# Kernel tuning notes

Hardware: AMD Instinct MI355X
Metric: run time of the kernel (lower is better)

The kernel has to match this reference:

```python
import jax, jax.numpy as jnp
import numpy as np

NEG_INF = jnp.float32(-(2.0**32) + 1.0)


def squash(z):
    # z: [B, k_max, out_units]
    sq_norm = jnp.sum(jnp.square(z), axis=-1, keepdims=True)
    scale = sq_norm / (1.0 + sq_norm) / jnp.sqrt(sq_norm + 1e-8)
    return scale * z


def setup_inputs() -> dict:
    key = jax.random.key(0)
    k1, k2, k3, k4 = jax.random.split(key, 4)
    B, L, D_IN, D_OUT, K = 1024, 200, 256, 256, 8
    behavior_embeddings = jax.random.normal(k1, (B, L, D_IN), dtype=jnp.float32)
    seq_len = jax.random.randint(k2, (B, 1), 1, L + 1, dtype=jnp.int32)
    routing_logits = jax.random.normal(k3, (1, K, L), dtype=jnp.float32)  # init_std=1.0
    bilinear_mapping_matrix = jax.random.normal(k4, (D_IN, D_OUT), dtype=jnp.float32)
    return {
        "behavior_embeddings": behavior_embeddings,
        "seq_len": seq_len,
        "routing_logits": routing_logits,
        "bilinear_mapping_matrix": bilinear_mapping_matrix,
    }


def reference(behavior_embeddings, seq_len, routing_logits, bilinear_mapping_matrix):
    ITERATION_TIMES = 3
    B, L, _ = behavior_embeddings.shape
    K = routing_logits.shape[1]

    # mask: [B, 1, L] broadcastable to [B, K, L] (same seq_len for every capsule)
    mask = jnp.arange(L)[None, None, :] < seq_len[:, :, None]

    # bilinear map is loop-invariant: [B, L, out_units]
    mapped = jnp.einsum("ble,eo->blo", behavior_embeddings, bilinear_mapping_matrix)

    logits = routing_logits  # [1, K, L]
    interest_capsules = None
    for _ in range(ITERATION_TIMES):
        logits_pad = jnp.where(mask, jnp.broadcast_to(logits, (B, K, L)), NEG_INF)
        weight = jax.nn.softmax(logits_pad, axis=-1)          # [B, K, L]
        Z = jnp.einsum("bkl,blo->bko", weight, mapped)         # [B, K, out]
        interest_capsules = squash(Z)                          # [B, K, out]
        # delta: sum over batch of capsules @ mapped^T -> [1, K, L]
        delta = jnp.einsum("bko,blo->kl", interest_capsules, mapped)[None]
        logits = logits + delta  # emulates assign_add on non-trainable B

    return interest_capsules.reshape(-1, K, interest_capsules.shape[-1])
```

## Files before the change

kernel.cpp:

```cpp
#include <hip/hip_runtime.h>
#include <cstdint>
#include <cstddef>

#define B_    1024
#define L_    200
#define DIN_  256
#define DOUT_ 256
#define K_    8
#define M_    (B_ * L_)

typedef __attribute__((ext_vector_type(8))) short bf16x8;
typedef __attribute__((ext_vector_type(4))) float f32x4;

__device__ __forceinline__ float bf2f(unsigned short u) {
  union { unsigned int i; float f; } w; w.i = ((unsigned int)u) << 16; return w.f;
}
__device__ __forceinline__ unsigned short f2bf(float f) {
  union { float f; unsigned int i; } w; w.f = f;
  unsigned int x = w.i;
  return (unsigned short)((x + 0x7fffu + ((x >> 16) & 1u)) >> 16);
}

__global__ __launch_bounds__(256)
void wt_prep(const float* __restrict__ W, unsigned short* __restrict__ Wh,
             unsigned short* __restrict__ Wm, unsigned short* __restrict__ Wl)
{
  const int k = blockIdx.x;
  const int n = threadIdx.x;
  float x = W[k * DOUT_ + n];
  unsigned short h = f2bf(x);
  float r = x - bf2f(h);
  unsigned short m = f2bf(r);
  float r2 = r - bf2f(m);
  unsigned short l = f2bf(r2);
  const int k0b = k >> 5, quad = (k >> 3) & 3, j = k & 7;
  const int nt = n >> 4, lr = n & 15;
  const size_t idx = ((((size_t)k0b * 16 + nt) * 64) + (quad * 16 + lr)) * 8 + j;
  Wh[idx] = h;
  Wm[idx] = m;
  Wl[idx] = l;
}

__global__ __launch_bounds__(256, 2)
void gemm_mapped(const float* __restrict__ A,
                 const unsigned short* __restrict__ Wh,
                 const unsigned short* __restrict__ Wm,
                 const unsigned short* __restrict__ Wl,
                 float* __restrict__ C)
{
  const int t    = threadIdx.x;
  const int wave = t >> 6;
  const int lane = t & 63;
  const int quad = lane >> 4;
  const int lr   = lane & 15;
  const int m0   = blockIdx.x * 128 + wave * 32;

  f32x4 acc[2][16];
  #pragma unroll
  for (int mt = 0; mt < 2; ++mt)
    #pragma unroll
    for (int nt = 0; nt < 16; ++nt)
      acc[mt][nt] = (f32x4){0.f, 0.f, 0.f, 0.f};

  bf16x8 Bh[4], Bm[4], Bl[4];
  bf16x8 ah[2], am[2], al[2];
  float4 Af[2][2];

#define BLOAD(K0B, NT, S) do { \
    const size_t _off = (((size_t)(K0B) * 16 + (NT)) * 64 + lane) * 8; \
    Bh[S] = *(const bf16x8*)(Wh + _off); \
    Bm[S] = *(const bf16x8*)(Wm + _off); \
    Bl[S] = *(const bf16x8*)(Wl + _off); \
  } while (0)

  const float* ap0 = A + (size_t)(m0 + lr) * DIN_ + quad * 8;
  const float* ap1 = A + (size_t)(m0 + 16 + lr) * DIN_ + quad * 8;

  Af[0][0] = *(const float4*)(ap0);
  Af[0][1] = *(const float4*)(ap0 + 4);
  Af[1][0] = *(const float4*)(ap1);
  Af[1][1] = *(const float4*)(ap1 + 4);
  BLOAD(0, 0, 0); BLOAD(0, 1, 1); BLOAD(0, 2, 2); BLOAD(0, 3, 3);

  for (int k0b = 0; k0b < 8; ++k0b) {
    #pragma unroll
    for (int mt = 0; mt < 2; ++mt) {
      float xs[8] = {Af[mt][0].x, Af[mt][0].y, Af[mt][0].z, Af[mt][0].w,
                     Af[mt][1].x, Af[mt][1].y, Af[mt][1].z, Af[mt][1].w};
      #pragma unroll
      for (int j = 0; j < 8; ++j) {
        unsigned short h = f2bf(xs[j]);
        float r = xs[j] - bf2f(h);
        unsigned short mm = f2bf(r);
        float r2 = r - bf2f(mm);
        unsigned short ll = f2bf(r2);
        ah[mt][j] = (short)h; am[mt][j] = (short)mm; al[mt][j] = (short)ll;
      }
    }
    if (k0b < 7) {
      const int ko = (k0b + 1) * 32;
      Af[0][0] = *(const float4*)(ap0 + ko);
      Af[0][1] = *(const float4*)(ap0 + ko + 4);
      Af[1][0] = *(const float4*)(ap1 + ko);
      Af[1][1] = *(const float4*)(ap1 + ko + 4);
    }

#define GROUP(NT, S) do { \
    f32x4 c0 = acc[0][NT], c1 = acc[1][NT]; \
    c0 = __builtin_amdgcn_mfma_f32_16x16x32_bf16(ah[0], Bh[S], c0, 0, 0, 0); \
    c1 = __builtin_amdgcn_mfma_f32_16x16x32_bf16(ah[1], Bh[S], c1, 0, 0, 0); \
    c0 = __builtin_amdgcn_mfma_f32_16x16x32_bf16(ah[0], Bm[S], c0, 0, 0, 0); \
    c1 = __builtin_amdgcn_mfma_f32_16x16x32_bf16(ah[1], Bm[S], c1, 0, 0, 0); \
    c0 = __builtin_amdgcn_mfma_f32_16x16x32_bf16(am[0], Bh[S], c0, 0, 0, 0); \
    c1 = __builtin_amdgcn_mfma_f32_16x16x32_bf16(am[1], Bh[S], c1, 0, 0, 0); \
    c0 = __builtin_amdgcn_mfma_f32_16x16x32_bf16(ah[0], Bl[S], c0, 0, 0, 0); \
    c1 = __builtin_amdgcn_mfma_f32_16x16x32_bf16(ah[1], Bl[S], c1, 0, 0, 0); \
    c0 = __builtin_amdgcn_mfma_f32_16x16x32_bf16(am[0], Bm[S], c0, 0, 0, 0); \
    c1 = __builtin_amdgcn_mfma_f32_16x16x32_bf16(am[1], Bm[S], c1, 0, 0, 0); \
    c0 = __builtin_amdgcn_mfma_f32_16x16x32_bf16(al[0], Bh[S], c0, 0, 0, 0); \
    c1 = __builtin_amdgcn_mfma_f32_16x16x32_bf16(al[1], Bh[S], c1, 0, 0, 0); \
    acc[0][NT] = c0; acc[1][NT] = c1; \
  } while (0)

    GROUP(0, 0);  BLOAD(k0b, 4, 0);
    GROUP(1, 1);  BLOAD(k0b, 5, 1);
    GROUP(2, 2);  BLOAD(k0b, 6, 2);
    GROUP(3, 3);  BLOAD(k0b, 7, 3);
    GROUP(4, 0);  BLOAD(k0b, 8, 0);
    GROUP(5, 1);  BLOAD(k0b, 9, 1);
    GROUP(6, 2);  BLOAD(k0b, 10, 2);
    GROUP(7, 3);  BLOAD(k0b, 11, 3);
    GROUP(8, 0);  BLOAD(k0b, 12, 0);
    GROUP(9, 1);  BLOAD(k0b, 13, 1);
    GROUP(10, 2); BLOAD(k0b, 14, 2);
    GROUP(11, 3); BLOAD(k0b, 15, 3);
    GROUP(12, 0);
    GROUP(13, 1);
    GROUP(14, 2);
    GROUP(15, 3);
    if (k0b < 7) {
      BLOAD(k0b + 1, 0, 0); BLOAD(k0b + 1, 1, 1);
      BLOAD(k0b + 1, 2, 2); BLOAD(k0b + 1, 3, 3);
    }
#undef GROUP
  }
#undef BLOAD

  #pragma unroll
  for (int mt = 0; mt < 2; ++mt)
    #pragma unroll
    for (int nt = 0; nt < 16; ++nt)
      #pragma unroll
      for (int r = 0; r < 4; ++r) {
        int row = m0 + mt * 16 + quad * 4 + r;
        C[(size_t)row * DOUT_ + nt * 16 + lr] = acc[mt][nt][r];
      }
}

#define DSCALE     67108864.0f
#define DSCALE_INV 1.4901161193847656e-8f

__global__ __launch_bounds__(256, 4)
void z_soft(const float* __restrict__ mapped,
            const float* __restrict__ rlog,
            const long long* __restrict__ accA,
            const long long* __restrict__ accB,
            const int* __restrict__ seq_len,
            float* __restrict__ caps)
{
  const int t    = threadIdx.x;
  const int lane = t & 63;
  const int wave = t >> 6;
  const int b    = blockIdx.x;
  const int len  = seq_len[b];

  __shared__ float wsmT[200][8];
  __shared__ float zred[2][8][256];
  __shared__ float sqred[4][8];

  #pragma unroll
  for (int kk = 0; kk < 2; ++kk) {
    const int k = wave * 2 + kk;
    float v[4];
    float mx = -3.4028235e38f;
    #pragma unroll
    for (int i = 0; i < 4; ++i) {
      int l = lane + 64 * i;
      float lv = -3.4028235e38f;
      if (l < len) {
        long long a = accA[(k * L_ + l) * 8] + accB[(k * L_ + l) * 8];
        lv = rlog[k * L_ + l] + (float)a * DSCALE_INV;
      }
      v[i] = lv;
      mx = fmaxf(mx, lv);
    }
    #pragma unroll
    for (int s = 1; s < 64; s <<= 1) mx = fmaxf(mx, __shfl_xor(mx, s, 64));
    float e[4]; float sum = 0.f;
    #pragma unroll
    for (int i = 0; i < 4; ++i) {
      int l = lane + 64 * i;
      e[i] = (l < len) ? __expf(v[i] - mx) : 0.f;
      sum += e[i];
    }
    #pragma unroll
    for (int s = 1; s < 64; s <<= 1) sum += __shfl_xor(sum, s, 64);
    float inv = 1.f / sum;
    #pragma unroll
    for (int i = 0; i < 4; ++i) {
      int l = lane + 64 * i;
      if (l < L_) wsmT[l][k] = e[i] * inv;
    }
  }
  __syncthreads();

  f32x4 zacc[K_];
  #pragma unroll
  for (int k = 0; k < K_; ++k) zacc[k] = (f32x4){0.f, 0.f, 0.f, 0.f};

  const float* mp = mapped + (size_t)b * (L_ * DOUT_) + lane * 4;
  for (int l = wave; l < len; l += 4) {
    f32x4 m = *(const f32x4*)(mp + (size_t)l * DOUT_);
    float4 w0 = *(const float4*)&wsmT[l][0];
    float4 w1 = *(const float4*)&wsmT[l][4];
    zacc[0] += w0.x * m; zacc[1] += w0.y * m;
    zacc[2] += w0.z * m; zacc[3] += w0.w * m;
    zacc[4] += w1.x * m; zacc[5] += w1.y * m;
    zacc[6] += w1.z * m; zacc[7] += w1.w * m;
  }

  if (wave >= 2) {
    #pragma unroll
    for (int k = 0; k < K_; ++k)
      *(f32x4*)&zred[wave - 2][k][lane * 4] = zacc[k];
  }
  __syncthreads();
  if (wave < 2) {
    #pragma unroll
    for (int k = 0; k < K_; ++k) {
      f32x4 r = *(const f32x4*)&zred[wave][k][lane * 4];
      r += zacc[k];
      *(f32x4*)&zred[wave][k][lane * 4] = r;
    }
  }
  __syncthreads();

  float z[K_];
  #pragma unroll
  for (int k = 0; k < K_; ++k) z[k] = zred[0][k][t] + zred[1][k][t];

  #pragma unroll
  for (int k = 0; k < K_; ++k) {
    float s2 = z[k] * z[k];
    #pragma unroll
    for (int s = 1; s < 64; s <<= 1) s2 += __shfl_xor(s2, s, 64);
    if (lane == 0) sqred[wave][k] = s2;
  }
  __syncthreads();
  #pragma unroll
  for (int k = 0; k < K_; ++k) {
    float sq = sqred[0][k] + sqred[1][k] + sqred[2][k] + sqred[3][k];
    float scale = sq / ((1.f + sq) * sqrtf(sq + 1e-8f));
    caps[((size_t)b * K_ + k) * DOUT_ + t] = scale * z[k];
  }
}

__global__ __launch_bounds__(256)
void delta_kernel(const float* __restrict__ mapped, const float* __restrict__ caps,
                  long long* __restrict__ accOut)
{
  const int t    = threadIdx.x;
  const int lane = t & 63;
  const int wave = t >> 6;
  const int wid  = blockIdx.x * 4 + wave;
  const int lc   = wid % 50;
  const int bc   = wid / 50;
  const int l0   = lc * 4;
  const int o4   = lane * 4;

  const float* cb = caps   + (size_t)(bc * 16) * (K_ * DOUT_) + o4;
  const float* mb = mapped + ((size_t)(bc * 16) * L_ + l0) * DOUT_ + o4;

  float acc[K_][4];
  #pragma unroll
  for (int k = 0; k < K_; ++k)
    #pragma unroll
    for (int ll = 0; ll < 4; ++ll) acc[k][ll] = 0.f;

  float4 cA[K_], mA[4], cB[K_], mB[4];

#define LOADC(DST, BI) do { \
    const float* _p = cb + (size_t)(BI) * (K_ * DOUT_); \
    _Pragma("unroll") \
    for (int _k = 0; _k < K_; ++_k) DST[_k] = *(const float4*)(_p + _k * DOUT_); \
  } while (0)
#define LOADM(DST, BI) do { \
    const float* _p = mb + (size_t)(BI) * (L_ * DOUT_); \
    _Pragma("unroll") \
    for (int _l = 0; _l < 4; ++_l) DST[_l] = *(const float4*)(_p + _l * DOUT_); \
  } while (0)
#define COMPUTE(CC, MM) do { \
    _Pragma("unroll") \
    for (int _k = 0; _k < K_; ++_k) \
      _Pragma("unroll") \
      for (int _l = 0; _l < 4; ++_l) \
        acc[_k][_l] += CC[_k].x * MM[_l].x + CC[_k].y * MM[_l].y \
                     + CC[_k].z * MM[_l].z + CC[_k].w * MM[_l].w; \
  } while (0)

  LOADC(cA, 0); LOADM(mA, 0);
  for (int i = 0; i < 8; ++i) {
    LOADC(cB, 2 * i + 1); LOADM(mB, 2 * i + 1);
    COMPUTE(cA, mA);
    if (i < 7) { LOADC(cA, 2 * i + 2); LOADM(mA, 2 * i + 2); }
    COMPUTE(cB, mB);
  }
#undef LOADC
#undef LOADM
#undef COMPUTE

  float out = 0.f;
  #pragma unroll
  for (int k = 0; k < K_; ++k)
    #pragma unroll
    for (int ll = 0; ll < 4; ++ll) {
      float v = acc[k][ll];
      v += __shfl_xor(v, 1, 64);
      v += __shfl_xor(v, 2, 64);
      v += __shfl_xor(v, 4, 64);
      v += __shfl_xor(v, 8, 64);
      v += __shfl_xor(v, 16, 64);
      v += __shfl_xor(v, 32, 64);
      if (lane == k * 4 + ll) out = v;
    }
  if (lane < 32) {
    long long q = llrintf(out * DSCALE);
    atomicAdd((unsigned long long*)&accOut[((size_t)(lane >> 2) * L_ + l0 + (lane & 3)) * 8],
              (unsigned long long)q);
  }
}

__global__ __launch_bounds__(256)
void init_acc(long long* __restrict__ a)
{
  int i = blockIdx.x * 256 + threadIdx.x;
  a[i] = 0;
}

extern "C" void kernel_launch(void* const* d_in, const int* in_sizes, int n_in,
                              void* d_out, int out_size, void* d_ws, size_t ws_size,
                              hipStream_t stream)
{
  const float* behav = (const float*)d_in[0];
  const int*   slen  = (const int*)d_in[1];
  const float* rlog  = (const float*)d_in[2];
  const float* W     = (const float*)d_in[3];
  float* caps = (float*)d_out;

  char* ws = (char*)d_ws;
  long long* z0   = (long long*)ws;
  long long* acc0 = (long long*)(ws + 102400);
  long long* acc1 = (long long*)(ws + 204800);
  unsigned short* Wh = (unsigned short*)(ws + 327680);
  unsigned short* Wm = (unsigned short*)(ws + 458752);
  unsigned short* Wl = (unsigned short*)(ws + 589824);
  float* mapped   = (float*)(ws + (1 << 20));

  init_acc<<<dim3(150), 256, 0, stream>>>((long long*)ws);
  wt_prep<<<dim3(256), 256, 0, stream>>>(W, Wh, Wm, Wl);
  gemm_mapped<<<dim3(1600), 256, 0, stream>>>(behav, Wh, Wm, Wl, mapped);

  z_soft<<<dim3(B_), 256, 0, stream>>>(mapped, rlog, z0,   z0,   slen, caps);
  delta_kernel<<<dim3(800), 256, 0, stream>>>(mapped, caps, acc0);
  z_soft<<<dim3(B_), 256, 0, stream>>>(mapped, rlog, acc0, z0,   slen, caps);
  delta_kernel<<<dim3(800), 256, 0, stream>>>(mapped, caps, acc1);
  z_soft<<<dim3(B_), 256, 0, stream>>>(mapped, rlog, acc0, acc1, slen, caps);
}
```

Baseline: 606.1 us.

## Stage split-bf16 weight tiles in LDS via async loads and split N across waves

The GEMM now loads each K-slice of the three bf16 weight splits into shared memory with global_load_lds, shared by all four waves, instead of each wave reading B directly from global memory. Waves are now split 2x2 over M and N, so each wave computes 32 rows by 128 columns, the block covers 64 rows, and the grid doubles. This cuts redundant global and L2 traffic for the weights and lowers accumulator registers so occupancy can rise. The cost is a full barrier with vmcnt(0) per K-step and no double buffering, so load latency is exposed, and the A-side conversion work is duplicated across the two N-halves.

```diff
diff --git a/kernel.cpp b/kernel.cpp
--- a/kernel.cpp
+++ b/kernel.cpp
@@ -19,6 +19,12 @@
   union { float f; unsigned int i; } w; w.f = f;
   unsigned int x = w.i;
   return (unsigned short)((x + 0x7fffu + ((x >> 16) & 1u)) >> 16);
+}
+
+__device__ __forceinline__ void gload16(const void* g, void* l) {
+  __builtin_amdgcn_global_load_lds(
+      (const __attribute__((address_space(1))) unsigned int*)g,
+      (__attribute__((address_space(3))) unsigned int*)l, 16, 0, 0);
 }
 
 __global__ __launch_bounds__(256)
@@ -41,7 +47,7 @@
   Wl[idx] = l;
 }
 
-__global__ __launch_bounds__(256, 2)
+__global__ __launch_bounds__(256, 3)
 void gemm_mapped(const float* __restrict__ A,
                  const unsigned short* __restrict__ Wh,
                  const unsigned short* __restrict__ Wm,
@@ -53,34 +59,41 @@
   const int lane = t & 63;
   const int quad = lane >> 4;
   const int lr   = lane & 15;
-  const int m0   = blockIdx.x * 128 + wave * 32;
-
-  f32x4 acc[2][16];
+  const int m0   = blockIdx.x * 64 + (wave & 1) * 32;
+  const int nt0  = (wave >> 1) * 8;
+
+  __shared__ unsigned short ldsB[3 * 16 * 64 * 8];
+
+  f32x4 acc[2][8];
   #pragma unroll
   for (int mt = 0; mt < 2; ++mt)
     #pragma unroll
-    for (int nt = 0; nt < 16; ++nt)
+    for (int nt = 0; nt < 8; ++nt)
       acc[mt][nt] = (f32x4){0.f, 0.f, 0.f, 0.f};
 
-  bf16x8 Bh[4], Bm[4], Bl[4];
   bf16x8 ah[2], am[2], al[2];
   float4 Af[2][2];
 
-#define BLOAD(K0B, NT, S) do { \
-    const size_t _off = (((size_t)(K0B) * 16 + (NT)) * 64 + lane) * 8; \
-    Bh[S] = *(const bf16x8*)(Wh + _off); \
-    Bm[S] = *(const bf16x8*)(Wm + _off); \
-    Bl[S] = *(const bf16x8*)(Wl + _off); \
-  } while (0)
-
   const float* ap0 = A + (size_t)(m0 + lr) * DIN_ + quad * 8;
   const float* ap1 = A + (size_t)(m0 + 16 + lr) * DIN_ + quad * 8;
+
+#define STAGE(K0B) do { \
+    const size_t _k = (size_t)(K0B) * 8192; \
+    _Pragma("unroll") \
+    for (int _r = 0; _r < 4; ++_r) { \
+      gload16(Wh + _k + _r * 2048 + t * 8, ldsB +         _r * 2048 + t * 8); \
+      gload16(Wm + _k + _r * 2048 + t * 8, ldsB +  8192 + _r * 2048 + t * 8); \
+      gload16(Wl + _k + _r * 2048 + t * 8, ldsB + 16384 + _r * 2048 + t * 8); \
+    } \
+  } while (0)
 
   Af[0][0] = *(const float4*)(ap0);
   Af[0][1] = *(const float4*)(ap0 + 4);
   Af[1][0] = *(const float4*)(ap1);
   Af[1][1] = *(const float4*)(ap1 + 4);
-  BLOAD(0, 0, 0); BLOAD(0, 1, 1); BLOAD(0, 2, 2); BLOAD(0, 3, 3);
+  STAGE(0);
+  asm volatile("s_waitcnt vmcnt(0)" ::: "memory");
+  __syncthreads();
 
   for (int k0b = 0; k0b < 8; ++k0b) {
     #pragma unroll
@@ -105,55 +118,48 @@
       Af[1][1] = *(const float4*)(ap1 + ko + 4);
     }
 
-#define GROUP(NT, S) do { \
+#define GROUP(NT) do { \
+    const unsigned short* _lb = ldsB + (size_t)((nt0 + (NT)) * 64 + lane) * 8; \
+    bf16x8 Bh_ = *(const bf16x8*)(_lb); \
+    bf16x8 Bm_ = *(const bf16x8*)(_lb + 8192); \
+    bf16x8 Bl_ = *(const bf16x8*)(_lb + 16384); \
     f32x4 c0 = acc[0][NT], c1 = acc[1][NT]; \
-    c0 = __builtin_amdgcn_mfma_f32_16x16x32_bf16(ah[0], Bh[S], c0, 0, 0, 0); \
-    c1 = __builtin_amdgcn_mfma_f32_16x16x32_bf16(ah[1], Bh[S], c1, 0, 0, 0); \
-    c0 = __builtin_amdgcn_mfma_f32_16x16x32_bf16(ah[0], Bm[S], c0, 0, 0, 0); \
-    c1 = __builtin_amdgcn_mfma_f32_16x16x32_bf16(ah[1], Bm[S], c1, 0, 0, 0); \
-    c0 = __builtin_amdgcn_mfma_f32_16x16x32_bf16(am[0], Bh[S], c0, 0, 0, 0); \
-    c1 = __builtin_amdgcn_mfma_f32_16x16x32_bf16(am[1], Bh[S], c1, 0, 0, 0); \
-    c0 = __builtin_amdgcn_mfma_f32_16x16x32_bf16(ah[0], Bl[S], c0, 0, 0, 0); \
-    c1 = __builtin_amdgcn_mfma_f32_16x16x32_bf16(ah[1], Bl[S], c1, 0, 0, 0); \
-    c0 = __builtin_amdgcn_mfma_f32_16x16x32_bf16(am[0], Bm[S], c0, 0, 0, 0); \
-    c1 = __builtin_amdgcn_mfma_f32_16x16x32_bf16(am[1], Bm[S], c1, 0, 0, 0); \
-    c0 = __builtin_amdgcn_mfma_f32_16x16x32_bf16(al[0], Bh[S], c0, 0, 0, 0); \
-    c1 = __builtin_amdgcn_mfma_f32_16x16x32_bf16(al[1], Bh[S], c1, 0, 0, 0); \
+    c0 = __builtin_amdgcn_mfma_f32_16x16x32_bf16(ah[0], Bh_, c0, 0, 0, 0); \
+    c1 = __builtin_amdgcn_mfma_f32_16x16x32_bf16(ah[1], Bh_, c1, 0, 0, 0); \
+    c0 = __builtin_amdgcn_mfma_f32_16x16x32_bf16(ah[0], Bm_, c0, 0, 0, 0); \
+    c1 = __builtin_amdgcn_mfma_f32_16x16x32_bf16(ah[1], Bm_, c1, 0, 0, 0); \
+    c0 = __builtin_amdgcn_mfma_f32_16x16x32_bf16(am[0], Bh_, c0, 0, 0, 0); \
+    c1 = __builtin_amdgcn_mfma_f32_16x16x32_bf16(am[1], Bh_, c1, 0, 0, 0); \
+    c0 = __builtin_amdgcn_mfma_f32_16x16x32_bf16(ah[0], Bl_, c0, 0, 0, 0); \
+    c1 = __builtin_amdgcn_mfma_f32_16x16x32_bf16(ah[1], Bl_, c1, 0, 0, 0); \
+    c0 = __builtin_amdgcn_mfma_f32_16x16x32_bf16(am[0], Bm_, c0, 0, 0, 0); \
+    c1 = __builtin_amdgcn_mfma_f32_16x16x32_bf16(am[1], Bm_, c1, 0, 0, 0); \
+    c0 = __builtin_amdgcn_mfma_f32_16x16x32_bf16(al[0], Bh_, c0, 0, 0, 0); \
+    c1 = __builtin_amdgcn_mfma_f32_16x16x32_bf16(al[1], Bh_, c1, 0, 0, 0); \
     acc[0][NT] = c0; acc[1][NT] = c1; \
   } while (0)
 
-    GROUP(0, 0);  BLOAD(k0b, 4, 0);
-    GROUP(1, 1);  BLOAD(k0b, 5, 1);
-    GROUP(2, 2);  BLOAD(k0b, 6, 2);
-    GROUP(3, 3);  BLOAD(k0b, 7, 3);
-    GROUP(4, 0);  BLOAD(k0b, 8, 0);
-    GROUP(5, 1);  BLOAD(k0b, 9, 1);
-    GROUP(6, 2);  BLOAD(k0b, 10, 2);
-    GROUP(7, 3);  BLOAD(k0b, 11, 3);
-    GROUP(8, 0);  BLOAD(k0b, 12, 0);
-    GROUP(9, 1);  BLOAD(k0b, 13, 1);
-    GROUP(10, 2); BLOAD(k0b, 14, 2);
-    GROUP(11, 3); BLOAD(k0b, 15, 3);
-    GROUP(12, 0);
-    GROUP(13, 1);
-    GROUP(14, 2);
-    GROUP(15, 3);
+    GROUP(0); GROUP(1); GROUP(2); GROUP(3);
+    GROUP(4); GROUP(5); GROUP(6); GROUP(7);
+#undef GROUP
+
+    __syncthreads();
     if (k0b < 7) {
-      BLOAD(k0b + 1, 0, 0); BLOAD(k0b + 1, 1, 1);
-      BLOAD(k0b + 1, 2, 2); BLOAD(k0b + 1, 3, 3);
-    }
-#undef GROUP
-  }
-#undef BLOAD
+      STAGE(k0b + 1);
+      asm volatile("s_waitcnt vmcnt(0)" ::: "memory");
+      __syncthreads();
+    }
+  }
+#undef STAGE
 
   #pragma unroll
   for (int mt = 0; mt < 2; ++mt)
     #pragma unroll
-    for (int nt = 0; nt < 16; ++nt)
+    for (int nt = 0; nt < 8; ++nt)
       #pragma unroll
       for (int r = 0; r < 4; ++r) {
         int row = m0 + mt * 16 + quad * 4 + r;
-        C[(size_t)row * DOUT_ + nt * 16 + lr] = acc[mt][nt][r];
+        C[(size_t)row * DOUT_ + (nt0 + nt) * 16 + lr] = acc[mt][nt][r];
       }
 }
 
@@ -368,7 +374,7 @@
 
   init_acc<<<dim3(150), 256, 0, stream>>>((long long*)ws);
   wt_prep<<<dim3(256), 256, 0, stream>>>(W, Wh, Wm, Wl);
-  gemm_mapped<<<dim3(1600), 256, 0, stream>>>(behav, Wh, Wm, Wl, mapped);
+  gemm_mapped<<<dim3(3200), 256, 0, stream>>>(behav, Wh, Wm, Wl, mapped);
 
   z_soft<<<dim3(B_), 256, 0, stream>>>(mapped, rlog, z0,   z0,   slen, caps);
   delta_kernel<<<dim3(800), 256, 0, stream>>>(mapped, caps, acc0);
```

After: 578.1 us. -4.6%, faster.
